# Kernel optimization log

Hardware: AMD Instinct MI355X
Metric: run time of the kernel (lower is better)

The kernel has to match this reference:

```python
import jax, jax.numpy as jnp
import numpy as np

B, C, D = 16, 512, 256
K = 16        # spatio_topk
RD = 128      # rec_dim
H = 8         # num_heads
FFN = 1024    # temporal_ffn
TEMP = 0.5    # temperature


def setup_inputs() -> dict:
    key = jax.random.key(0)
    ks = jax.random.split(key, 8)
    s = lambda k, shape: (jax.random.normal(k, shape, jnp.float32) * 0.02)
    return dict(
        x=jax.random.normal(ks[0], (B, C, D), jnp.float32),
        wq_rec=s(ks[1], (RD, D)),
        wk_rec=s(ks[2], (RD, D)),
        in_proj_w=s(ks[3], (3 * D, D)),
        in_proj_b=jnp.zeros((3 * D,), jnp.float32),
        out_w=s(ks[4], (D, D)),
        out_b=jnp.zeros((D,), jnp.float32),
        ln1_g=jnp.ones((D,), jnp.float32),
        ln1_b=jnp.zeros((D,), jnp.float32),
        mlp_w1=s(ks[5], (FFN, D)),
        mlp_b1=jnp.zeros((FFN,), jnp.float32),
        mlp_w2=s(ks[6], (D, FFN)),
        mlp_b2=jnp.zeros((D,), jnp.float32),
        ln2_g=jnp.ones((D,), jnp.float32),
        ln2_b=jnp.zeros((D,), jnp.float32),
    )


def _ln(x, g, b, eps=1e-5):
    m = x.mean(-1, keepdims=True)
    v = ((x - m) ** 2).mean(-1, keepdims=True)
    return (x - m) * jax.lax.rsqrt(v + eps) * g + b


def reference(x, wq_rec, wk_rec, in_proj_w, in_proj_b, out_w, out_b,
              ln1_g, ln1_b, mlp_w1, mlp_b1, mlp_w2, mlp_b2, ln2_g, ln2_b):
    b, c, d = x.shape
    # --- ST_Rec_Module (training branch: straight-through top-k routing) ---
    xq = x @ wq_rec.T                                   # (B,C,RD)
    xk = x @ wk_rec.T
    logits = jnp.einsum('bqd,bkd->bqk', xq, xk) / TEMP  # (B,C,C)
    idx = jax.lax.top_k(logits, K)[1]                   # (B,C,K)
    z_hard = jax.nn.one_hot(idx, c, dtype=x.dtype)      # (B,C,K,C)
    # cumulative mask of previously-selected channels (exclusive cumsum)
    prev = jnp.cumsum(z_hard, axis=2)
    prev = jnp.concatenate([jnp.zeros_like(prev[:, :, :1]), prev[:, :, :-1]], axis=2)
    mask = prev > 0
    zs = jnp.where(mask, -1e30, logits[:, :, None, :] / TEMP)  # logits/temp twice, as in source
    z_soft = jax.nn.softmax(zs, axis=-1)
    z = z_hard + z_soft - jax.lax.stop_gradient(z_soft)        # straight-through
    rec_x = jnp.einsum('bqkc,bcd->bqkd', z, x)                 # (B,C,K,D)

    # --- ST_Channel_Module: per-channel cross-attention, query length 1 ---
    hd = d // H
    wq, wk, wv = in_proj_w[:d], in_proj_w[d:2 * d], in_proj_w[2 * d:]
    bq, bk, bv = in_proj_b[:d], in_proj_b[d:2 * d], in_proj_b[2 * d:]
    q = (x @ wq.T + bq).reshape(b, c, H, hd)                   # (B,C,H,hd)
    k = (rec_x @ wk.T + bk).reshape(b, c, K, H, hd)
    v = (rec_x @ wv.T + bv).reshape(b, c, K, H, hd)
    scores = jnp.einsum('bchd,bckhd->bchk', q, k) / np.float32(np.sqrt(hd))
    attn = jax.nn.softmax(scores, axis=-1)
    ctx = jnp.einsum('bchk,bckhd->bchd', attn, v).reshape(b, c, d)
    attn_out = ctx @ out_w.T + out_b
    x1 = _ln(attn_out + x, ln1_g, ln1_b)

    # --- ST_Temporal_Module (Identity projections, gelu FFN + LN) ---
    h = jax.nn.gelu(x1 @ mlp_w1.T + mlp_b1, approximate=False)
    h = h @ mlp_w2.T + mlp_b2
    x2 = _ln(h + x1, ln2_g, ln2_b)
    return x2
```

## Files before the change

kernel.cpp:

```cpp
#include <hip/hip_runtime.h>
#include <hip/hip_bf16.h>
#include <math.h>

#define B_   16
#define C_   512
#define D_   256
#define K_   16
#define RD_  128
#define H_   8
#define HD_  32
#define FFN_ 1024
#define M_   (B_ * C_)

typedef __attribute__((ext_vector_type(8))) short bf16x8;
typedef __attribute__((ext_vector_type(4))) float f32x4;

typedef __attribute__((address_space(1))) const int ga_int;
typedef __attribute__((address_space(3))) int ls_int;

static __device__ __forceinline__ short f2bf(float v) {
    __hip_bfloat16 h = __float2bfloat16(v);
    return *(short*)&h;
}
static __device__ __forceinline__ float bf2f(short s) {
    __hip_bfloat16 h = *(__hip_bfloat16*)&s;
    return __bfloat162float(h);
}
static __device__ __forceinline__ float4 ld4bf(const short* p) {
    uint2 u = *(const uint2*)p;
    float4 r;
    r.x = __uint_as_float((u.x & 0xffffu) << 16);
    r.y = __uint_as_float(u.x & 0xffff0000u);
    r.z = __uint_as_float((u.y & 0xffffu) << 16);
    r.w = __uint_as_float(u.y & 0xffff0000u);
    return r;
}

#define N8_X    (M_ * D_ / 8)
#define N8_INW  (768 * D_ / 8)
#define N8_OUTW (D_ * D_ / 8)
#define N8_W1   (FFN_ * D_ / 8)
#define N8_W2   (D_ * FFN_ / 8)
#define N8_WQ   (RD_ * D_ / 8)
#define N8_ALL  (N8_X + N8_INW + N8_OUTW + N8_W1 + N8_W2 + 2 * N8_WQ)

__global__ __launch_bounds__(256) void convert_all_kernel(
    const float* __restrict__ x, const float* __restrict__ inw,
    const float* __restrict__ outw, const float* __restrict__ w1,
    const float* __restrict__ w2, const float* __restrict__ wq,
    const float* __restrict__ wk,
    short* __restrict__ xbf, short* __restrict__ xlo,
    short* __restrict__ inwbf, short* __restrict__ outwbf,
    short* __restrict__ w1bf, short* __restrict__ w2bf,
    short* __restrict__ wqh, short* __restrict__ wql,
    short* __restrict__ wkh, short* __restrict__ wkl)
{
    int i = blockIdx.x * 256 + threadIdx.x;
    if (i >= N8_ALL) return;

    const float* s; short* dh; short* dl = nullptr; int off;
    if      (i < N8_X)                    { s = x;    dh = xbf;    dl = xlo; off = i; }
    else if (i < N8_X + N8_INW)           { s = inw;  dh = inwbf;  off = i - N8_X; }
    else if (i < N8_X + N8_INW + N8_OUTW) { s = outw; dh = outwbf; off = i - N8_X - N8_INW; }
    else if (i < N8_X + N8_INW + N8_OUTW + N8_W1)
                                          { s = w1;   dh = w1bf;   off = i - N8_X - N8_INW - N8_OUTW; }
    else if (i < N8_X + N8_INW + N8_OUTW + N8_W1 + N8_W2)
                                          { s = w2;   dh = w2bf;   off = i - N8_X - N8_INW - N8_OUTW - N8_W1; }
    else if (i < N8_X + N8_INW + N8_OUTW + N8_W1 + N8_W2 + N8_WQ)
                                          { s = wq;   dh = wqh; dl = wql; off = i - N8_X - N8_INW - N8_OUTW - N8_W1 - N8_W2; }
    else                                  { s = wk;   dh = wkh; dl = wkl; off = i - N8_X - N8_INW - N8_OUTW - N8_W1 - N8_W2 - N8_WQ; }

    const float4* sp = (const float4*)s + (size_t)off * 2;
    float4 v0 = sp[0], v1 = sp[1];
    float f[8] = {v0.x, v0.y, v0.z, v0.w, v1.x, v1.y, v1.z, v1.w};
    short rh[8], rl[8];
    #pragma unroll
    for (int j = 0; j < 8; ++j) {
        rh[j] = f2bf(f[j]);
        rl[j] = f2bf(f[j] - bf2f(rh[j]));
    }
    *(bf16x8*)(dh + (size_t)off * 8) = *(bf16x8*)rh;
    if (dl) *(bf16x8*)(dl + (size_t)off * 8) = *(bf16x8*)rl;
}

template<int BM, int BN, int OUT_BF16, int ACT>
__global__ __launch_bounds__(256) void gemm_mfma(
    const short* __restrict__ A, const short* __restrict__ W,
    const float* __restrict__ bias, void* __restrict__ Cout,
    int M, int N, int Kd)
{
    __shared__ short As[2][BM * 32];
    __shared__ short Bs[2][BN * 32];
    const int tid  = threadIdx.x;
    const int wave = tid >> 6;
    const int lane = tid & 63;
    const int bm = blockIdx.y * BM;
    const int bn = blockIdx.x * BN;
    constexpr int MI = BM / 32;
    constexpr int NJ = BN / 32;
    const int wr = (wave >> 1) * (BM / 2);
    const int wc = (wave & 1) * (BN / 2);

    const int fr = lane & 15;
    const int fk = (lane >> 4) * 8;
    const int r0 = tid >> 2, ch = (tid & 3) * 8;

    f32x4 acc[MI][NJ];
    #pragma unroll
    for (int i = 0; i < MI; ++i)
        #pragma unroll
        for (int j = 0; j < NJ; ++j)
            acc[i][j] = (f32x4){0.f, 0.f, 0.f, 0.f};

    auto stage = [&](int buf, int k0) {
        #pragma unroll
        for (int i = 0; i < BM / 64; ++i)
            __builtin_amdgcn_global_load_lds(
                (ga_int*)&A[(size_t)(bm + r0 + i * 64) * Kd + k0 + ch],
                (ls_int*)&As[buf][(tid + i * 256) * 8], 16, 0, 0);
        #pragma unroll
        for (int j = 0; j < BN / 64; ++j)
            __builtin_amdgcn_global_load_lds(
                (ga_int*)&W[(size_t)(bn + r0 + j * 64) * Kd + k0 + ch],
                (ls_int*)&Bs[buf][(tid + j * 256) * 8], 16, 0, 0);
    };

    stage(0, 0);
    int cur = 0;

    for (int k0 = 0; k0 < Kd; k0 += 32) {
        __syncthreads();
        if (k0 + 32 < Kd) stage(cur ^ 1, k0 + 32);

        bf16x8 af[MI], bfr[NJ];
        #pragma unroll
        for (int i = 0; i < MI; ++i) af[i]  = *(bf16x8*)&As[cur][(wr + i * 16 + fr) * 32 + fk];
        #pragma unroll
        for (int j = 0; j < NJ; ++j) bfr[j] = *(bf16x8*)&Bs[cur][(wc + j * 16 + fr) * 32 + fk];
        #pragma unroll
        for (int i = 0; i < MI; ++i)
            #pragma unroll
            for (int j = 0; j < NJ; ++j)
                acc[i][j] = __builtin_amdgcn_mfma_f32_16x16x32_bf16(af[i], bfr[j], acc[i][j], 0, 0, 0);
        cur ^= 1;
    }

    const int rowbase = (lane >> 4) * 4;
    #pragma unroll
    for (int i = 0; i < MI; ++i) {
        #pragma unroll
        for (int j = 0; j < NJ; ++j) {
            const int n = bn + wc + j * 16 + fr;
            const float bn_v = bias ? bias[n] : 0.f;
            #pragma unroll
            for (int r = 0; r < 4; ++r) {
                const int m = bm + wr + i * 16 + rowbase + r;
                float v = acc[i][j][r] + bn_v;
                if (ACT) v = 0.5f * v * (1.0f + erff(v * 0.70710678118654752f));
                if (OUT_BF16) ((short*)Cout)[(size_t)m * N + n] = f2bf(v);
                else          ((float*)Cout)[(size_t)m * N + n] = v;
            }
        }
    }
}

template<int KD, int WBF>
__global__ __launch_bounds__(256) void gemm_ln_mfma(
    const short* __restrict__ A, const short* __restrict__ W,
    const float* __restrict__ bias, const float* __restrict__ res,
    const float* __restrict__ g, const float* __restrict__ beta,
    float* __restrict__ out, short* __restrict__ outbf)
{
    __shared__ short As[2][32 * 32];
    __shared__ short Bs[2][256 * 32];
    __shared__ float part[4][32][2];

    const int tid  = threadIdx.x;
    const int wave = tid >> 6;
    const int lane = tid & 63;
    const int bm = blockIdx.x * 32;
    const int wc = wave * 64;
    const int fr = lane & 15;
    const int fk = (lane >> 4) * 8;
    const int r0 = tid >> 2, ch = (tid & 3) * 8;

    f32x4 acc[2][4];
    #pragma unroll
    for (int i = 0; i < 2; ++i)
        #pragma unroll
        for (int j = 0; j < 4; ++j)
            acc[i][j] = (f32x4){0.f, 0.f, 0.f, 0.f};

    auto stage = [&](int buf, int k0) {
        if (tid < 128)
            __builtin_amdgcn_global_load_lds(
                (ga_int*)&A[(size_t)(bm + r0) * KD + k0 + ch],
                (ls_int*)&As[buf][tid * 8], 16, 0, 0);
        #pragma unroll
        for (int j = 0; j < 4; ++j)
            __builtin_amdgcn_global_load_lds(
                (ga_int*)&W[(size_t)(r0 + j * 64) * KD + k0 + ch],
                (ls_int*)&Bs[buf][(tid + j * 256) * 8], 16, 0, 0);
    };

    stage(0, 0);
    int cur = 0;

    for (int k0 = 0; k0 < KD; k0 += 32) {
        __syncthreads();
        if (k0 + 32 < KD) stage(cur ^ 1, k0 + 32);

        bf16x8 af[2], bfr[4];
        #pragma unroll
        for (int i = 0; i < 2; ++i) af[i]  = *(bf16x8*)&As[cur][(i * 16 + fr) * 32 + fk];
        #pragma unroll
        for (int j = 0; j < 4; ++j) bfr[j] = *(bf16x8*)&Bs[cur][(wc + j * 16 + fr) * 32 + fk];
        #pragma unroll
        for (int i = 0; i < 2; ++i)
            #pragma unroll
            for (int j = 0; j < 4; ++j)
                acc[i][j] = __builtin_amdgcn_mfma_f32_16x16x32_bf16(af[i], bfr[j], acc[i][j], 0, 0, 0);
        cur ^= 1;
    }

    const int rowbase = (lane >> 4) * 4;
    float vv[2][4][4];
    float sum[2][4], sq[2][4];
    #pragma unroll
    for (int i = 0; i < 2; ++i)
        #pragma unroll
        for (int r = 0; r < 4; ++r) { sum[i][r] = 0.f; sq[i][r] = 0.f; }

    #pragma unroll
    for (int i = 0; i < 2; ++i)
        #pragma unroll
        for (int j = 0; j < 4; ++j) {
            const int n = wc + j * 16 + fr;
            const float bv = bias[n];
            #pragma unroll
            for (int r = 0; r < 4; ++r) {
                const int m = bm + i * 16 + rowbase + r;
                float v = acc[i][j][r] + bv + res[(size_t)m * D_ + n];
                vv[i][j][r] = v;
                sum[i][r] += v;
                sq[i][r]  += v * v;
            }
        }

    #pragma unroll
    for (int i = 0; i < 2; ++i)
        #pragma unroll
        for (int r = 0; r < 4; ++r)
            #pragma unroll
            for (int s = 1; s < 16; s <<= 1) {
                sum[i][r] += __shfl_xor(sum[i][r], s, 64);
                sq[i][r]  += __shfl_xor(sq[i][r],  s, 64);
            }

    if (fr == 0) {
        #pragma unroll
        for (int i = 0; i < 2; ++i)
            #pragma unroll
            for (int r = 0; r < 4; ++r) {
                int ml = i * 16 + rowbase + r;
                part[wave][ml][0] = sum[i][r];
                part[wave][ml][1] = sq[i][r];
            }
    }
    __syncthreads();

    #pragma unroll
    for (int i = 0; i < 2; ++i)
        #pragma unroll
        for (int r = 0; r < 4; ++r) {
            const int ml = i * 16 + rowbase + r;
            const float S = part[0][ml][0] + part[1][ml][0] + part[2][ml][0] + part[3][ml][0];
            const float Q = part[0][ml][1] + part[1][ml][1] + part[2][ml][1] + part[3][ml][1];
            const float mean = S * (1.0f / D_);
            const float var  = Q * (1.0f / D_) - mean * mean;
            const float rstd = rsqrtf(var + 1e-5f);
            const int m = bm + ml;
            #pragma unroll
            for (int j = 0; j < 4; ++j) {
                const int n = wc + j * 16 + fr;
                float o = (vv[i][j][r] - mean) * rstd * g[n] + beta[n];
                out[(size_t)m * D_ + n] = o;
                if (WBF) outbf[(size_t)m * D_ + n] = f2bf(o);
            }
        }
}

__global__ __launch_bounds__(256) void xqk_mfma(
    const short* __restrict__ xh, const short* __restrict__ xl,
    const short* __restrict__ wqh, const short* __restrict__ wql,
    const short* __restrict__ wkh, const short* __restrict__ wkl,
    short* __restrict__ qh, short* __restrict__ ql,
    short* __restrict__ kh, short* __restrict__ kl)
{
    __shared__ short Ah[64 * 32], Al[64 * 32], Bh[64 * 32], Bl[64 * 32];
    const short* Wh = blockIdx.z ? wkh : wqh;
    const short* Wl = blockIdx.z ? wkl : wql;
    short* Oh       = blockIdx.z ? kh : qh;
    short* Ol       = blockIdx.z ? kl : ql;

    const int tid  = threadIdx.x;
    const int wave = tid >> 6;
    const int lane = tid & 63;
    const int bm = blockIdx.y * 64;
    const int bn = blockIdx.x * 64;
    const int wr = (wave >> 1) * 32;
    const int wc = (wave & 1) * 32;
    const int fr = lane & 15;
    const int fk = (lane >> 4) * 8;
    const int r0 = tid >> 2, ch = (tid & 3) * 8;

    f32x4 acc[2][2];
    #pragma unroll
    for (int i = 0; i < 2; ++i)
        #pragma unroll
        for (int j = 0; j < 2; ++j)
            acc[i][j] = (f32x4){0.f, 0.f, 0.f, 0.f};

    for (int k0 = 0; k0 < D_; k0 += 32) {
        __builtin_amdgcn_global_load_lds((ga_int*)&xh[(size_t)(bm + r0) * D_ + k0 + ch], (ls_int*)&Ah[tid * 8], 16, 0, 0);
        __builtin_amdgcn_global_load_lds((ga_int*)&xl[(size_t)(bm + r0) * D_ + k0 + ch], (ls_int*)&Al[tid * 8], 16, 0, 0);
        __builtin_amdgcn_global_load_lds((ga_int*)&Wh[(size_t)(bn + r0) * D_ + k0 + ch], (ls_int*)&Bh[tid * 8], 16, 0, 0);
        __builtin_amdgcn_global_load_lds((ga_int*)&Wl[(size_t)(bn + r0) * D_ + k0 + ch], (ls_int*)&Bl[tid * 8], 16, 0, 0);
        __syncthreads();

        bf16x8 ah[2], al[2], bh[2], bl[2];
        #pragma unroll
        for (int i = 0; i < 2; ++i) {
            ah[i] = *(bf16x8*)&Ah[(wr + i * 16 + fr) * 32 + fk];
            al[i] = *(bf16x8*)&Al[(wr + i * 16 + fr) * 32 + fk];
        }
        #pragma unroll
        for (int j = 0; j < 2; ++j) {
            bh[j] = *(bf16x8*)&Bh[(wc + j * 16 + fr) * 32 + fk];
            bl[j] = *(bf16x8*)&Bl[(wc + j * 16 + fr) * 32 + fk];
        }
        #pragma unroll
        for (int i = 0; i < 2; ++i)
            #pragma unroll
            for (int j = 0; j < 2; ++j) {
                acc[i][j] = __builtin_amdgcn_mfma_f32_16x16x32_bf16(ah[i], bh[j], acc[i][j], 0, 0, 0);
                acc[i][j] = __builtin_amdgcn_mfma_f32_16x16x32_bf16(ah[i], bl[j], acc[i][j], 0, 0, 0);
                acc[i][j] = __builtin_amdgcn_mfma_f32_16x16x32_bf16(al[i], bh[j], acc[i][j], 0, 0, 0);
            }
        __syncthreads();
    }

    const int rowbase = (lane >> 4) * 4;
    #pragma unroll
    for (int i = 0; i < 2; ++i)
        #pragma unroll
        for (int j = 0; j < 2; ++j) {
            const int n = bn + wc + j * 16 + fr;
            #pragma unroll
            for (int r = 0; r < 4; ++r) {
                const int m = bm + wr + i * 16 + rowbase + r;
                float v = acc[i][j][r];
                short h = f2bf(v);
                Oh[(size_t)m * RD_ + n] = h;
                Ol[(size_t)m * RD_ + n] = f2bf(v - bf2f(h));
            }
        }
}

__global__ __launch_bounds__(256) void logits_mfma(
    const short* __restrict__ qh, const short* __restrict__ ql,
    const short* __restrict__ kh, const short* __restrict__ kl,
    float* __restrict__ out)
{
    __shared__ short Ah[64 * 32], Al[64 * 32], Bh[64 * 32], Bl[64 * 32];
    const int tid  = threadIdx.x;
    const int wave = tid >> 6;
    const int lane = tid & 63;
    const int base = blockIdx.z * C_;
    const int bm = blockIdx.y * 64;
    const int bn = blockIdx.x * 64;
    const int wr = (wave >> 1) * 32;
    const int wc = (wave & 1) * 32;
    const int fr = lane & 15;
    const int fk = (lane >> 4) * 8;
    const int r0 = tid >> 2, ch = (tid & 3) * 8;

    f32x4 acc[2][2];
    #pragma unroll
    for (int i = 0; i < 2; ++i)
        #pragma unroll
        for (int j = 0; j < 2; ++j)
            acc[i][j] = (f32x4){0.f, 0.f, 0.f, 0.f};

    for (int k0 = 0; k0 < RD_; k0 += 32) {
        __builtin_amdgcn_global_load_lds((ga_int*)&qh[(size_t)(base + bm + r0) * RD_ + k0 + ch], (ls_int*)&Ah[tid * 8], 16, 0, 0);
        __builtin_amdgcn_global_load_lds((ga_int*)&ql[(size_t)(base + bm + r0) * RD_ + k0 + ch], (ls_int*)&Al[tid * 8], 16, 0, 0);
        __builtin_amdgcn_global_load_lds((ga_int*)&kh[(size_t)(base + bn + r0) * RD_ + k0 + ch], (ls_int*)&Bh[tid * 8], 16, 0, 0);
        __builtin_amdgcn_global_load_lds((ga_int*)&kl[(size_t)(base + bn + r0) * RD_ + k0 + ch], (ls_int*)&Bl[tid * 8], 16, 0, 0);
        __syncthreads();

        bf16x8 ah[2], al[2], bh[2], bl[2];
        #pragma unroll
        for (int i = 0; i < 2; ++i) {
            ah[i] = *(bf16x8*)&Ah[(wr + i * 16 + fr) * 32 + fk];
            al[i] = *(bf16x8*)&Al[(wr + i * 16 + fr) * 32 + fk];
        }
        #pragma unroll
        for (int j = 0; j < 2; ++j) {
            bh[j] = *(bf16x8*)&Bh[(wc + j * 16 + fr) * 32 + fk];
            bl[j] = *(bf16x8*)&Bl[(wc + j * 16 + fr) * 32 + fk];
        }
        #pragma unroll
        for (int i = 0; i < 2; ++i)
            #pragma unroll
            for (int j = 0; j < 2; ++j) {
                acc[i][j] = __builtin_amdgcn_mfma_f32_16x16x32_bf16(ah[i], bh[j], acc[i][j], 0, 0, 0);
                acc[i][j] = __builtin_amdgcn_mfma_f32_16x16x32_bf16(ah[i], bl[j], acc[i][j], 0, 0, 0);
                acc[i][j] = __builtin_amdgcn_mfma_f32_16x16x32_bf16(al[i], bh[j], acc[i][j], 0, 0, 0);
            }
        __syncthreads();
    }

    const int rowbase = (lane >> 4) * 4;
    #pragma unroll
    for (int i = 0; i < 2; ++i)
        #pragma unroll
        for (int j = 0; j < 2; ++j) {
            const int n = bn + wc + j * 16 + fr;
            #pragma unroll
            for (int r = 0; r < 4; ++r) {
                const int m = base + bm + wr + i * 16 + rowbase + r;
                out[(size_t)m * C_ + n] = acc[i][j][r];
            }
        }
}

__global__ __launch_bounds__(256) void topk_attn_kernel(
    const float* __restrict__ logits, const short* __restrict__ qkv,
    short* __restrict__ ctxbf)
{
    const int wave = threadIdx.x >> 6;
    const int lane = threadIdx.x & 63;
    const int row  = blockIdx.x * 4 + wave;
    const int bbase = row & ~(C_ - 1);

    const float* lrow = logits + (size_t)row * C_;
    unsigned long long key[8];
    #pragma unroll
    for (int j = 0; j < 8; ++j) {
        int pos = lane * 8 + j;
        unsigned u = __float_as_uint(lrow[pos]);
        u = (u & 0x80000000u) ? ~u : (u | 0x80000000u);
        key[j] = (((unsigned long long)u) << 9) | (unsigned)(511 - pos);
    }

    int ii[K_];
    #pragma unroll
    for (int sel = 0; sel < K_; ++sel) {
        unsigned long long best = key[0];
        #pragma unroll
        for (int j = 1; j < 8; ++j) best = key[j] > best ? key[j] : best;
        #pragma unroll
        for (int s = 1; s < 64; s <<= 1) {
            unsigned long long o = __shfl_xor(best, s, 64);
            best = o > best ? o : best;
        }
        int pos = 511 - (int)(best & 511ull);
        ii[sel] = pos;
        if ((pos >> 3) == lane) key[pos & 7] = 0ull;
    }

    const short* qrow = qkv + (size_t)row * 768;
    float4 qv = ld4bf(qrow + lane * 4);

    float s[K_];
    #pragma unroll
    for (int k = 0; k < K_; ++k) {
        float4 kv = ld4bf(qkv + (size_t)(bbase + ii[k]) * 768 + 256 + lane * 4);
        float p = qv.x * kv.x + qv.y * kv.y + qv.z * kv.z + qv.w * kv.w;
        p += __shfl_xor(p, 1, 64);
        p += __shfl_xor(p, 2, 64);
        p += __shfl_xor(p, 4, 64);
        s[k] = p * 0.17677669529663687f;
    }

    float m = s[0];
    #pragma unroll
    for (int k = 1; k < K_; ++k) m = fmaxf(m, s[k]);
    float ssum = 0.f;
    #pragma unroll
    for (int k = 0; k < K_; ++k) { s[k] = __expf(s[k] - m); ssum += s[k]; }
    const float inv = 1.f / ssum;

    float4 acc = {0.f, 0.f, 0.f, 0.f};
    #pragma unroll
    for (int k = 0; k < K_; ++k) {
        float4 vvv = ld4bf(qkv + (size_t)(bbase + ii[k]) * 768 + 512 + lane * 4);
        float w = s[k] * inv;
        acc.x += w * vvv.x; acc.y += w * vvv.y; acc.z += w * vvv.z; acc.w += w * vvv.w;
    }

    unsigned lo = (unsigned)(unsigned short)f2bf(acc.x) | ((unsigned)(unsigned short)f2bf(acc.y) << 16);
    unsigned hi = (unsigned)(unsigned short)f2bf(acc.z) | ((unsigned)(unsigned short)f2bf(acc.w) << 16);
    uint2 pk = {lo, hi};
    *(uint2*)(ctxbf + (size_t)row * D_ + lane * 4) = pk;
}

extern "C" void kernel_launch(void* const* d_in, const int* in_sizes, int n_in,
                              void* d_out, int out_size, void* d_ws, size_t ws_size,
                              hipStream_t stream)
{
    const float* x      = (const float*)d_in[0];
    const float* wq_rec = (const float*)d_in[1];
    const float* wk_rec = (const float*)d_in[2];
    const float* in_w   = (const float*)d_in[3];
    const float* in_b   = (const float*)d_in[4];
    const float* out_w  = (const float*)d_in[5];
    const float* out_b  = (const float*)d_in[6];
    const float* ln1_g  = (const float*)d_in[7];
    const float* ln1_b  = (const float*)d_in[8];
    const float* w1     = (const float*)d_in[9];
    const float* b1     = (const float*)d_in[10];
    const float* w2     = (const float*)d_in[11];
    const float* b2     = (const float*)d_in[12];
    const float* ln2_g  = (const float*)d_in[13];
    const float* ln2_b  = (const float*)d_in[14];
    float* out = (float*)d_out;

    short* qkvbf = (short*)d_ws;
    short* qh    = qkvbf + (size_t)M_ * 768;
    short* ql    = qh + (size_t)M_ * RD_;
    short* kh    = ql + (size_t)M_ * RD_;
    short* kl    = kh + (size_t)M_ * RD_;
    float* x1    = (float*)(kl + (size_t)M_ * RD_);
    float* U     = x1 + (size_t)M_ * D_;
    float* logits = U;
    short* ctxbf  = (short*)(U + (size_t)M_ * 512);
    short* x1bf   = ctxbf + (size_t)M_ * D_;
    short* hbf    = x1bf  + (size_t)M_ * D_;
    short* xbf    = hbf   + (size_t)M_ * FFN_;
    short* xlo    = xbf   + (size_t)M_ * D_;
    short* inwbf  = xlo   + (size_t)M_ * D_;
    short* outwbf = inwbf + (size_t)768 * D_;
    short* w1bf   = outwbf + (size_t)D_ * D_;
    short* w2bf   = w1bf  + (size_t)FFN_ * D_;
    short* wqh    = w2bf  + (size_t)D_ * FFN_;
    short* wql    = wqh + (size_t)RD_ * D_;
    short* wkh    = wql + (size_t)RD_ * D_;
    short* wkl    = wkh + (size_t)RD_ * D_;

    dim3 blk(256);

    convert_all_kernel<<<dim3((N8_ALL + 255) / 256), blk, 0, stream>>>(
        x, in_w, out_w, w1, w2, wq_rec, wk_rec,
        xbf, xlo, inwbf, outwbf, w1bf, w2bf, wqh, wql, wkh, wkl);

    gemm_mfma<64, 128, 1, 0><<<dim3(768 / 128, M_ / 64), blk, 0, stream>>>(xbf, inwbf, in_b, qkvbf, M_, 768, D_);
    xqk_mfma<<<dim3(RD_ / 64, M_ / 64, 2), blk, 0, stream>>>(
        xbf, xlo, wqh, wql, wkh, wkl, qh, ql, kh, kl);
    logits_mfma<<<dim3(C_ / 64, C_ / 64, B_), blk, 0, stream>>>(qh, ql, kh, kl, logits);
    topk_attn_kernel<<<dim3(M_ / 4), blk, 0, stream>>>(logits, qkvbf, ctxbf);
    gemm_ln_mfma<256, 1><<<dim3(M_ / 32), blk, 0, stream>>>(
        ctxbf, outwbf, out_b, x, ln1_g, ln1_b, x1, x1bf);
    gemm_mfma<128, 128, 1, 1><<<dim3(FFN_ / 128, M_ / 128), blk, 0, stream>>>(x1bf, w1bf, b1, hbf, M_, FFN_, D_);
    gemm_ln_mfma<1024, 0><<<dim3(M_ / 32), blk, 0, stream>>>(
        hbf, w2bf, b2, x1, ln2_g, ln2_b, out, nullptr);
}
```

Before: 123.1 us.

## Merge projection kernels, shrink LN-GEMM row tiles, and simplify top-k selection

The QKV projection GEMM and the hi/lo split recurrent-projection GEMM now run as one launch that branches on block id, removing a launch and letting both fill the GPU together. The fused GEMM+LayerNorm kernel drops its row tile from 32 to 16 to double the block count. The FFN1 GEMM switches to a 64-row tile for the same reason. Top-k selection now does a float max-reduce with a ballot to find the winning lane instead of a 64-bit packed-key reduce, which cuts shuffle traffic but relies on ballot ordering for ties.

```diff
diff --git a/kernel.cpp b/kernel.cpp
--- a/kernel.cpp
+++ b/kernel.cpp
@@ -164,207 +164,151 @@
     }
 }
 
-template<int KD, int WBF>
-__global__ __launch_bounds__(256) void gemm_ln_mfma(
-    const short* __restrict__ A, const short* __restrict__ W,
-    const float* __restrict__ bias, const float* __restrict__ res,
-    const float* __restrict__ g, const float* __restrict__ beta,
-    float* __restrict__ out, short* __restrict__ outbf)
+__global__ __launch_bounds__(256) void proj_kernel(
+    const short* __restrict__ xbf, const short* __restrict__ xlo,
+    const short* __restrict__ inwbf, const float* __restrict__ in_b,
+    const short* __restrict__ wqh, const short* __restrict__ wql,
+    const short* __restrict__ wkh, const short* __restrict__ wkl,
+    short* __restrict__ qkvbf,
+    short* __restrict__ qh, short* __restrict__ ql,
+    short* __restrict__ kh, short* __restrict__ kl)
 {
-    __shared__ short As[2][32 * 32];
-    __shared__ short Bs[2][256 * 32];
-    __shared__ float part[4][32][2];
-
+    __shared__ short smem[12288];
+    const int bid  = blockIdx.x;
     const int tid  = threadIdx.x;
     const int wave = tid >> 6;
     const int lane = tid & 63;
-    const int bm = blockIdx.x * 32;
-    const int wc = wave * 64;
     const int fr = lane & 15;
     const int fk = (lane >> 4) * 8;
     const int r0 = tid >> 2, ch = (tid & 3) * 8;
 
-    f32x4 acc[2][4];
-    #pragma unroll
-    for (int i = 0; i < 2; ++i)
-        #pragma unroll
-        for (int j = 0; j < 4; ++j)
-            acc[i][j] = (f32x4){0.f, 0.f, 0.f, 0.f};
-
-    auto stage = [&](int buf, int k0) {
-        if (tid < 128)
+    if (bid < 768) {
+        const int bm = (bid / 6) * 64;
+        const int bn = (bid % 6) * 128;
+        const int wr = (wave >> 1) * 32;
+        const int wc = (wave & 1) * 64;
+        short* As = smem;
+        short* Bs = smem + 4096;
+
+        f32x4 acc[2][4];
+        #pragma unroll
+        for (int i = 0; i < 2; ++i)
+            #pragma unroll
+            for (int j = 0; j < 4; ++j)
+                acc[i][j] = (f32x4){0.f, 0.f, 0.f, 0.f};
+
+        auto stage = [&](int buf, int k0) {
             __builtin_amdgcn_global_load_lds(
-                (ga_int*)&A[(size_t)(bm + r0) * KD + k0 + ch],
-                (ls_int*)&As[buf][tid * 8], 16, 0, 0);
-        #pragma unroll
-        for (int j = 0; j < 4; ++j)
-            __builtin_amdgcn_global_load_lds(
-                (ga_int*)&W[(size_t)(r0 + j * 64) * KD + k0 + ch],
-                (ls_int*)&Bs[buf][(tid + j * 256) * 8], 16, 0, 0);
-    };
-
-    stage(0, 0);
-    int cur = 0;
-
-    for (int k0 = 0; k0 < KD; k0 += 32) {
-        __syncthreads();
-        if (k0 + 32 < KD) stage(cur ^ 1, k0 + 32);
-
-        bf16x8 af[2], bfr[4];
-        #pragma unroll
-        for (int i = 0; i < 2; ++i) af[i]  = *(bf16x8*)&As[cur][(i * 16 + fr) * 32 + fk];
-        #pragma unroll
-        for (int j = 0; j < 4; ++j) bfr[j] = *(bf16x8*)&Bs[cur][(wc + j * 16 + fr) * 32 + fk];
+                (ga_int*)&xbf[(size_t)(bm + r0) * D_ + k0 + ch],
+                (ls_int*)&As[buf * 2048 + tid * 8], 16, 0, 0);
+            #pragma unroll
+            for (int j = 0; j < 2; ++j)
+                __builtin_amdgcn_global_load_lds(
+                    (ga_int*)&inwbf[(size_t)(bn + r0 + j * 64) * D_ + k0 + ch],
+                    (ls_int*)&Bs[buf * 4096 + (tid + j * 256) * 8], 16, 0, 0);
+        };
+
+        stage(0, 0);
+        int cur = 0;
+        for (int k0 = 0; k0 < D_; k0 += 32) {
+            __syncthreads();
+            if (k0 + 32 < D_) stage(cur ^ 1, k0 + 32);
+            bf16x8 af[2], bfr[4];
+            #pragma unroll
+            for (int i = 0; i < 2; ++i) af[i]  = *(bf16x8*)&As[cur * 2048 + (wr + i * 16 + fr) * 32 + fk];
+            #pragma unroll
+            for (int j = 0; j < 4; ++j) bfr[j] = *(bf16x8*)&Bs[cur * 4096 + (wc + j * 16 + fr) * 32 + fk];
+            #pragma unroll
+            for (int i = 0; i < 2; ++i)
+                #pragma unroll
+                for (int j = 0; j < 4; ++j)
+                    acc[i][j] = __builtin_amdgcn_mfma_f32_16x16x32_bf16(af[i], bfr[j], acc[i][j], 0, 0, 0);
+            cur ^= 1;
+        }
+
+        const int rowbase = (lane >> 4) * 4;
         #pragma unroll
         for (int i = 0; i < 2; ++i)
             #pragma unroll
-            for (int j = 0; j < 4; ++j)
-                acc[i][j] = __builtin_amdgcn_mfma_f32_16x16x32_bf16(af[i], bfr[j], acc[i][j], 0, 0, 0);
-        cur ^= 1;
-    }
-
-    const int rowbase = (lane >> 4) * 4;
-    float vv[2][4][4];
-    float sum[2][4], sq[2][4];
-    #pragma unroll
-    for (int i = 0; i < 2; ++i)
-        #pragma unroll
-        for (int r = 0; r < 4; ++r) { sum[i][r] = 0.f; sq[i][r] = 0.f; }
-
-    #pragma unroll
-    for (int i = 0; i < 2; ++i)
-        #pragma unroll
-        for (int j = 0; j < 4; ++j) {
-            const int n = wc + j * 16 + fr;
-            const float bv = bias[n];
-            #pragma unroll
-            for (int r = 0; r < 4; ++r) {
-                const int m = bm + i * 16 + rowbase + r;
-                float v = acc[i][j][r] + bv + res[(size_t)m * D_ + n];
-                vv[i][j][r] = v;
-                sum[i][r] += v;
-                sq[i][r]  += v * v;
+            for (int j = 0; j < 4; ++j) {
+                const int n = bn + wc + j * 16 + fr;
+                const float bv = in_b[n];
+                #pragma unroll
+                for (int r = 0; r < 4; ++r) {
+                    const int m = bm + wr + i * 16 + rowbase + r;
+                    qkvbf[(size_t)m * 768 + n] = f2bf(acc[i][j][r] + bv);
+                }
             }
-        }
-
-    #pragma unroll
-    for (int i = 0; i < 2; ++i)
-        #pragma unroll
-        for (int r = 0; r < 4; ++r)
-            #pragma unroll
-            for (int s = 1; s < 16; s <<= 1) {
-                sum[i][r] += __shfl_xor(sum[i][r], s, 64);
-                sq[i][r]  += __shfl_xor(sq[i][r],  s, 64);
+    } else {
+        const int t = bid - 768;
+        const int z = t >> 8;
+        const int rem = t & 255;
+        const int bm = (rem >> 1) * 64;
+        const int bn = (rem & 1) * 64;
+        const short* Wh = z ? wkh : wqh;
+        const short* Wl = z ? wkl : wql;
+        short* Oh = z ? kh : qh;
+        short* Ol = z ? kl : ql;
+        short* Ah = smem;
+        short* Al = smem + 2048;
+        short* Bh = smem + 4096;
+        short* Bl = smem + 6144;
+
+        const int wr = (wave >> 1) * 32;
+        const int wc = (wave & 1) * 32;
+
+        f32x4 acc[2][2];
+        #pragma unroll
+        for (int i = 0; i < 2; ++i)
+            #pragma unroll
+            for (int j = 0; j < 2; ++j)
+                acc[i][j] = (f32x4){0.f, 0.f, 0.f, 0.f};
+
+        for (int k0 = 0; k0 < D_; k0 += 32) {
+            __builtin_amdgcn_global_load_lds((ga_int*)&xbf[(size_t)(bm + r0) * D_ + k0 + ch], (ls_int*)&Ah[tid * 8], 16, 0, 0);
+            __builtin_amdgcn_global_load_lds((ga_int*)&xlo[(size_t)(bm + r0) * D_ + k0 + ch], (ls_int*)&Al[tid * 8], 16, 0, 0);
+            __builtin_amdgcn_global_load_lds((ga_int*)&Wh[(size_t)(bn + r0) * D_ + k0 + ch], (ls_int*)&Bh[tid * 8], 16, 0, 0);
+            __builtin_amdgcn_global_load_lds((ga_int*)&Wl[(size_t)(bn + r0) * D_ + k0 + ch], (ls_int*)&Bl[tid * 8], 16, 0, 0);
+            __syncthreads();
+
+            bf16x8 ah[2], al[2], bh[2], bl[2];
+            #pragma unroll
+            for (int i = 0; i < 2; ++i) {
+                ah[i] = *(bf16x8*)&Ah[(wr + i * 16 + fr) * 32 + fk];
+                al[i] = *(bf16x8*)&Al[(wr + i * 16 + fr) * 32 + fk];
             }
-
-    if (fr == 0) {
+            #pragma unroll
+            for (int j = 0; j < 2; ++j) {
+                bh[j] = *(bf16x8*)&Bh[(wc + j * 16 + fr) * 32 + fk];
+                bl[j] = *(bf16x8*)&Bl[(wc + j * 16 + fr) * 32 + fk];
+            }
+            #pragma unroll
+            for (int i = 0; i < 2; ++i)
+                #pragma unroll
+                for (int j = 0; j < 2; ++j) {
+                    acc[i][j] = __builtin_amdgcn_mfma_f32_16x16x32_bf16(ah[i], bh[j], acc[i][j], 0, 0, 0);
+                    acc[i][j] = __builtin_amdgcn_mfma_f32_16x16x32_bf16(ah[i], bl[j], acc[i][j], 0, 0, 0);
+                    acc[i][j] = __builtin_amdgcn_mfma_f32_16x16x32_bf16(al[i], bh[j], acc[i][j], 0, 0, 0);
+                }
+            __syncthreads();
+        }
+
+        const int rowbase = (lane >> 4) * 4;
         #pragma unroll
         for (int i = 0; i < 2; ++i)
             #pragma unroll
-            for (int r = 0; r < 4; ++r) {
-                int ml = i * 16 + rowbase + r;
-                part[wave][ml][0] = sum[i][r];
-                part[wave][ml][1] = sq[i][r];
+            for (int j = 0; j < 2; ++j) {
+                const int n = bn + wc + j * 16 + fr;
+                #pragma unroll
+                for (int r = 0; r < 4; ++r) {
+                    const int m = bm + wr + i * 16 + rowbase + r;
+                    float v = acc[i][j][r];
+                    short h = f2bf(v);
+                    Oh[(size_t)m * RD_ + n] = h;
+                    Ol[(size_t)m * RD_ + n] = f2bf(v - bf2f(h));
+                }
             }
     }
-    __syncthreads();
-
-    #pragma unroll
-    for (int i = 0; i < 2; ++i)
-        #pragma unroll
-        for (int r = 0; r < 4; ++r) {
-            const int ml = i * 16 + rowbase + r;
-            const float S = part[0][ml][0] + part[1][ml][0] + part[2][ml][0] + part[3][ml][0];
-            const float Q = part[0][ml][1] + part[1][ml][1] + part[2][ml][1] + part[3][ml][1];
-            const float mean = S * (1.0f / D_);
-            const float var  = Q * (1.0f / D_) - mean * mean;
-            const float rstd = rsqrtf(var + 1e-5f);
-            const int m = bm + ml;
-            #pragma unroll
-            for (int j = 0; j < 4; ++j) {
-                const int n = wc + j * 16 + fr;
-                float o = (vv[i][j][r] - mean) * rstd * g[n] + beta[n];
-                out[(size_t)m * D_ + n] = o;
-                if (WBF) outbf[(size_t)m * D_ + n] = f2bf(o);
-            }
-        }
-}
-
-__global__ __launch_bounds__(256) void xqk_mfma(
-    const short* __restrict__ xh, const short* __restrict__ xl,
-    const short* __restrict__ wqh, const short* __restrict__ wql,
-    const short* __restrict__ wkh, const short* __restrict__ wkl,
-    short* __restrict__ qh, short* __restrict__ ql,
-    short* __restrict__ kh, short* __restrict__ kl)
-{
-    __shared__ short Ah[64 * 32], Al[64 * 32], Bh[64 * 32], Bl[64 * 32];
-    const short* Wh = blockIdx.z ? wkh : wqh;
-    const short* Wl = blockIdx.z ? wkl : wql;
-    short* Oh       = blockIdx.z ? kh : qh;
-    short* Ol       = blockIdx.z ? kl : ql;
-
-    const int tid  = threadIdx.x;
-    const int wave = tid >> 6;
-    const int lane = tid & 63;
-    const int bm = blockIdx.y * 64;
-    const int bn = blockIdx.x * 64;
-    const int wr = (wave >> 1) * 32;
-    const int wc = (wave & 1) * 32;
-    const int fr = lane & 15;
-    const int fk = (lane >> 4) * 8;
-    const int r0 = tid >> 2, ch = (tid & 3) * 8;
-
-    f32x4 acc[2][2];
-    #pragma unroll
-    for (int i = 0; i < 2; ++i)
-        #pragma unroll
-        for (int j = 0; j < 2; ++j)
-            acc[i][j] = (f32x4){0.f, 0.f, 0.f, 0.f};
-
-    for (int k0 = 0; k0 < D_; k0 += 32) {
-        __builtin_amdgcn_global_load_lds((ga_int*)&xh[(size_t)(bm + r0) * D_ + k0 + ch], (ls_int*)&Ah[tid * 8], 16, 0, 0);
-        __builtin_amdgcn_global_load_lds((ga_int*)&xl[(size_t)(bm + r0) * D_ + k0 + ch], (ls_int*)&Al[tid * 8], 16, 0, 0);
-        __builtin_amdgcn_global_load_lds((ga_int*)&Wh[(size_t)(bn + r0) * D_ + k0 + ch], (ls_int*)&Bh[tid * 8], 16, 0, 0);
-        __builtin_amdgcn_global_load_lds((ga_int*)&Wl[(size_t)(bn + r0) * D_ + k0 + ch], (ls_int*)&Bl[tid * 8], 16, 0, 0);
-        __syncthreads();
-
-        bf16x8 ah[2], al[2], bh[2], bl[2];
-        #pragma unroll
-        for (int i = 0; i < 2; ++i) {
-            ah[i] = *(bf16x8*)&Ah[(wr + i * 16 + fr) * 32 + fk];
-            al[i] = *(bf16x8*)&Al[(wr + i * 16 + fr) * 32 + fk];
-        }
-        #pragma unroll
-        for (int j = 0; j < 2; ++j) {
-            bh[j] = *(bf16x8*)&Bh[(wc + j * 16 + fr) * 32 + fk];
-            bl[j] = *(bf16x8*)&Bl[(wc + j * 16 + fr) * 32 + fk];
-        }
-        #pragma unroll
-        for (int i = 0; i < 2; ++i)
-            #pragma unroll
-            for (int j = 0; j < 2; ++j) {
-                acc[i][j] = __builtin_amdgcn_mfma_f32_16x16x32_bf16(ah[i], bh[j], acc[i][j], 0, 0, 0);
-                acc[i][j] = __builtin_amdgcn_mfma_f32_16x16x32_bf16(ah[i], bl[j], acc[i][j], 0, 0, 0);
-                acc[i][j] = __builtin_amdgcn_mfma_f32_16x16x32_bf16(al[i], bh[j], acc[i][j], 0, 0, 0);
-            }
-        __syncthreads();
-    }
-
-    const int rowbase = (lane >> 4) * 4;
-    #pragma unroll
-    for (int i = 0; i < 2; ++i)
-        #pragma unroll
-        for (int j = 0; j < 2; ++j) {
-            const int n = bn + wc + j * 16 + fr;
-            #pragma unroll
-            for (int r = 0; r < 4; ++r) {
-                const int m = bm + wr + i * 16 + rowbase + r;
-                float v = acc[i][j][r];
-                short h = f2bf(v);
-                Oh[(size_t)m * RD_ + n] = h;
-                Ol[(size_t)m * RD_ + n] = f2bf(v - bf2f(h));
-            }
-        }
 }
 
 __global__ __launch_bounds__(256) void logits_mfma(
@@ -445,29 +389,28 @@
     const int bbase = row & ~(C_ - 1);
 
     const float* lrow = logits + (size_t)row * C_;
-    unsigned long long key[8];
-    #pragma unroll
-    for (int j = 0; j < 8; ++j) {
-        int pos = lane * 8 + j;
-        unsigned u = __float_as_uint(lrow[pos]);
-        u = (u & 0x80000000u) ? ~u : (u | 0x80000000u);
-        key[j] = (((unsigned long long)u) << 9) | (unsigned)(511 - pos);
-    }
+    float v[8];
+    #pragma unroll
+    for (int j = 0; j < 8; ++j) v[j] = lrow[lane * 8 + j];
 
     int ii[K_];
     #pragma unroll
     for (int sel = 0; sel < K_; ++sel) {
-        unsigned long long best = key[0];
-        #pragma unroll
-        for (int j = 1; j < 8; ++j) best = key[j] > best ? key[j] : best;
-        #pragma unroll
-        for (int s = 1; s < 64; s <<= 1) {
-            unsigned long long o = __shfl_xor(best, s, 64);
-            best = o > best ? o : best;
-        }
-        int pos = 511 - (int)(best & 511ull);
-        ii[sel] = pos;
-        if ((pos >> 3) == lane) key[pos & 7] = 0ull;
+        float bv = v[0]; int bj = 0;
+        #pragma unroll
+        for (int j = 1; j < 8; ++j)
+            if (v[j] > bv) { bv = v[j]; bj = j; }
+        float wb = bv;
+        #pragma unroll
+        for (int s = 1; s < 64; s <<= 1)
+            wb = fmaxf(wb, __shfl_xor(wb, s, 64));
+        unsigned long long mask = __ballot(bv == wb);
+        int wl = __ffsll(mask) - 1;
+        int wj = __shfl(bj, wl, 64);
+        ii[sel] = wl * 8 + wj;
+        #pragma unroll
+        for (int j = 0; j < 8; ++j)
+            if (lane == wl && bj == j) v[j] = -INFINITY;
     }
 
     const short* qrow = qkv + (size_t)row * 768;
@@ -504,6 +447,114 @@
     unsigned hi = (unsigned)(unsigned short)f2bf(acc.z) | ((unsigned)(unsigned short)f2bf(acc.w) << 16);
     uint2 pk = {lo, hi};
     *(uint2*)(ctxbf + (size_t)row * D_ + lane * 4) = pk;
+}
+
+template<int KD, int WBF>
+__global__ __launch_bounds__(256) void gemm_ln_mfma(
+    const short* __restrict__ A, const short* __restrict__ W,
+    const float* __restrict__ bias, const float* __restrict__ res,
+    const float* __restrict__ g, const float* __restrict__ beta,
+    float* __restrict__ out, short* __restrict__ outbf)
+{
+    __shared__ short As[2][16 * 32];
+    __shared__ short Bs[2][256 * 32];
+    __shared__ float part[4][16][2];
+
+    const int tid  = threadIdx.x;
+    const int wave = tid >> 6;
+    const int lane = tid & 63;
+    const int bm = blockIdx.x * 16;
+    const int wc = wave * 64;
+    const int fr = lane & 15;
+    const int fk = (lane >> 4) * 8;
+    const int r0 = tid >> 2, ch = (tid & 3) * 8;
+
+    f32x4 acc[4];
+    #pragma unroll
+    for (int j = 0; j < 4; ++j) acc[j] = (f32x4){0.f, 0.f, 0.f, 0.f};
+
+    auto stage = [&](int buf, int k0) {
+        if (tid < 64)
+            __builtin_amdgcn_global_load_lds(
+                (ga_int*)&A[(size_t)(bm + r0) * KD + k0 + ch],
+                (ls_int*)&As[buf][tid * 8], 16, 0, 0);
+        #pragma unroll
+        for (int j = 0; j < 4; ++j)
+            __builtin_amdgcn_global_load_lds(
+                (ga_int*)&W[(size_t)(r0 + j * 64) * KD + k0 + ch],
+                (ls_int*)&Bs[buf][(tid + j * 256) * 8], 16, 0, 0);
+    };
+
+    stage(0, 0);
+    int cur = 0;
+
+    for (int k0 = 0; k0 < KD; k0 += 32) {
+        __syncthreads();
+        if (k0 + 32 < KD) stage(cur ^ 1, k0 + 32);
+
+        bf16x8 af = *(bf16x8*)&As[cur][fr * 32 + fk];
+        bf16x8 bfr[4];
+        #pragma unroll
+        for (int j = 0; j < 4; ++j) bfr[j] = *(bf16x8*)&Bs[cur][(wc + j * 16 + fr) * 32 + fk];
+        #pragma unroll
+        for (int j = 0; j < 4; ++j)
+            acc[j] = __builtin_amdgcn_mfma_f32_16x16x32_bf16(af, bfr[j], acc[j], 0, 0, 0);
+        cur ^= 1;
+    }
+
+    const int rowbase = (lane >> 4) * 4;
+    float vv[4][4];
+    float sum[4] = {0.f, 0.f, 0.f, 0.f};
+    float sq[4]  = {0.f, 0.f, 0.f, 0.f};
+
+    #pragma unroll
+    for (int j = 0; j < 4; ++j) {
+        const int n = wc + j * 16 + fr;
+        const float bv = bias[n];
+        #pragma unroll
+        for (int r = 0; r < 4; ++r) {
+            const int m = bm + rowbase + r;
+            float v = acc[j][r] + bv + res[(size_t)m * D_ + n];
+            vv[j][r] = v;
+            sum[r] += v;
+            sq[r]  += v * v;
+        }
+    }
+
+    #pragma unroll
+    for (int r = 0; r < 4; ++r)
+        #pragma unroll
+        for (int s = 1; s < 16; s <<= 1) {
+            sum[r] += __shfl_xor(sum[r], s, 64);
+            sq[r]  += __shfl_xor(sq[r],  s, 64);
+        }
+
+    if (fr == 0) {
+        #pragma unroll
+        for (int r = 0; r < 4; ++r) {
+            part[wave][rowbase + r][0] = sum[r];
+            part[wave][rowbase + r][1] = sq[r];
+        }
+    }
+    __syncthreads();
+
+    #pragma unroll
+    for (int r = 0; r < 4; ++r) {
+        const int ml = rowbase + r;
+        const float S = part[0][ml][0] + part[1][ml][0] + part[2][ml][0] + part[3][ml][0];
+        const float Q = part[0][ml][1] + part[1][ml][1] + part[2][ml][1] + part[3][ml][1];
+        const float mean = S * (1.0f / D_);
+        const float var  = Q * (1.0f / D_) - mean * mean;
+        const float rstd = rsqrtf(var + 1e-5f);
+        const int m = bm + ml;
+        #pragma unroll
+        for (int j = 0; j < 4; ++j) {
+            const int n = wc + j * 16 + fr;
+            float o = (vv[j][r] - mean) * rstd * g[n] + beta[n];
+            out[(size_t)m * D_ + n] = o;
+            if (WBF) outbf[(size_t)m * D_ + n] = f2bf(o);
+        }
+    }
 }
 
 extern "C" void kernel_launch(void* const* d_in, const int* in_sizes, int n_in,
@@ -555,14 +606,13 @@
         x, in_w, out_w, w1, w2, wq_rec, wk_rec,
         xbf, xlo, inwbf, outwbf, w1bf, w2bf, wqh, wql, wkh, wkl);
 
-    gemm_mfma<64, 128, 1, 0><<<dim3(768 / 128, M_ / 64), blk, 0, stream>>>(xbf, inwbf, in_b, qkvbf, M_, 768, D_);
-    xqk_mfma<<<dim3(RD_ / 64, M_ / 64, 2), blk, 0, stream>>>(
-        xbf, xlo, wqh, wql, wkh, wkl, qh, ql, kh, kl);
+    proj_kernel<<<dim3(1280), blk, 0, stream>>>(
+        xbf, xlo, inwbf, in_b, wqh, wql, wkh, wkl, qkvbf, qh, ql, kh, kl);
     logits_mfma<<<dim3(C_ / 64, C_ / 64, B_), blk, 0, stream>>>(qh, ql, kh, kl, logits);
     topk_attn_kernel<<<dim3(M_ / 4), blk, 0, stream>>>(logits, qkvbf, ctxbf);
-    gemm_ln_mfma<256, 1><<<dim3(M_ / 32), blk, 0, stream>>>(
+    gemm_ln_mfma<256, 1><<<dim3(M_ / 16), blk, 0, stream>>>(
         ctxbf, outwbf, out_b, x, ln1_g, ln1_b, x1, x1bf);
-    gemm_mfma<128, 128, 1, 1><<<dim3(FFN_ / 128, M_ / 128), blk, 0, stream>>>(x1bf, w1bf, b1, hbf, M_, FFN_, D_);
-    gemm_ln_mfma<1024, 0><<<dim3(M_ / 32), blk, 0, stream>>>(
+    gemm_mfma<64, 128, 1, 1><<<dim3(FFN_ / 128, M_ / 64), blk, 0, stream>>>(x1bf, w1bf, b1, hbf, M_, FFN_, D_);
+    gemm_ln_mfma<1024, 0><<<dim3(M_ / 16), blk, 0, stream>>>(
         hbf, w2bf, b2, x1, ln2_g, ln2_b, out, nullptr);
 }
```

New measurement: 106.3 us. -13.7%, faster.
